# Performance work log

Measured on AMD Instinct MI355X. Metric: run time of the kernel, lower is better.

## Reference

```python
import jax, jax.numpy as jnp
import numpy as np

EPS = 1e-5  # BatchNorm1d default eps


def _uf_death(fv, u, v):
    """0-dim lower-star persistence on a (disjoint-union) graph via union-find.
    fv: [N] vertex filtration values (float np). u, v: [E] endpoints (int np).
    Returns death[N]: index of the vertex whose filtration value is the death
    time of the component born at each vertex (self-index => essential / f,f).
    Edges are processed in order of their lower-star filtration value
    max(fv[u], fv[v]) (stable sort, matching simplex-tree filtration order).
    Elder rule: the component whose birth vertex has larger (f, index) dies.
    """
    N = fv.shape[0]
    fe = np.maximum(fv[u], fv[v])
    order = np.argsort(fe, kind='stable')
    parent = np.arange(N)
    birth = np.arange(N)   # birth vertex of the component rooted here
    death = np.arange(N)   # default: pair (f_v, f_v)

    def find(i):
        r = i
        while parent[r] != r:
            r = parent[r]
        while parent[i] != r:  # path compression
            parent[i], i = r, parent[i]
        return r

    for e in order:
        a, b = int(u[e]), int(v[e])
        ra, rb = find(a), find(b)
        if ra == rb:
            continue
        ba, bb = birth[ra], birth[rb]
        if (fv[ba], ba) <= (fv[bb], bb):
            elder_b, young_b = ba, bb
        else:
            elder_b, young_b = bb, ba
        # death vertex = edge endpoint realizing the edge filtration value
        w = a if (fv[a], a) >= (fv[b], b) else b
        death[young_b] = w
        parent[ra] = rb
        birth[rb] = elder_b
    return death


def _death_indices(x, W1, b1, W2, b2, edge_index):
    """Host-side (numpy) computation of pairing indices. Indices are piecewise
    constant w.r.t. the floats, so gradients do not flow through them."""
    xn = np.asarray(jax.device_get(x), dtype=np.float32)
    fv = np.maximum(xn @ np.asarray(W1) + np.asarray(b1), 0.0) @ np.asarray(W2) + np.asarray(b2)  # [N, F]
    ei = np.asarray(jax.device_get(edge_index))
    u, v = ei[0], ei[1]
    F = fv.shape[1]
    return np.stack([_uf_death(fv[:, k], u, v) for k in range(F)], axis=0)  # [F, N]


def _togl_forward(x, death_idx, batch, num_graphs,
                  W1, b1, W2, b2, W_in, b_in,
                  g1W, g1b, l1W, g2W, g2b, l2W, bn_gamma, bn_beta):
    N = x.shape[0]
    # Filtration MLP: Linear -> ReLU -> Linear
    fv = jnp.maximum(x @ W1 + b1, 0.0) @ W2 + b2          # [N, F]
    births = fv.T                                          # [F, N]
    deaths = jnp.take_along_axis(fv.T, death_idx, axis=1)  # [F, N]
    pd = jnp.stack([births, deaths], axis=-1)              # [F, N, 2]
    # per-node concat over filtrations: [N, 2F]
    x0 = pd.transpose(1, 0, 2).reshape(N, -1)
    x0 = jnp.maximum(x0 @ W_in + b_in, 0.0)                # Linear + ReLU

    def deepset(h, GW, Gb, LW):
        s = jax.ops.segment_sum(h, batch, num_segments=num_graphs)
        c = jax.ops.segment_sum(jnp.ones((h.shape[0], 1), h.dtype), batch,
                                num_segments=num_graphs)
        xm = (s / c) @ LW                                  # Lambda(scatter_mean)
        return h @ GW + Gb - xm[batch]

    x0 = jnp.maximum(deepset(x0, g1W, g1b, l1W), 0.0)      # DeepSet + ReLU
    x0 = deepset(x0, g2W, g2b, l2W)                        # DeepSet -> n_features
    r = jnp.maximum(x0, 0.0)
    mu = r.mean(axis=0)
    var = r.var(axis=0)                                    # biased, as BN training
    y = bn_gamma * (r - mu) * jax.lax.rsqrt(var + EPS) + bn_beta
    return x + y


def setup_inputs() -> dict:
    key = jax.random.key(0)
    ks = jax.random.split(key, 16)
    B, NPG, EPG = 32, 1024, 2048
    N, E = B * NPG, B * EPG
    n_feat, hid, n_filt, out_dim = 512, 512, 8, 64

    rng = np.random.default_rng(0)
    off = np.repeat(np.arange(B, dtype=np.int32) * NPG, EPG)
    u = rng.integers(0, NPG, E).astype(np.int32) + off
    v = rng.integers(0, NPG, E).astype(np.int32) + off
    edge_index = jnp.asarray(np.stack([u, v], axis=0))
    batch = jnp.asarray(np.repeat(np.arange(B, dtype=np.int32), NPG))
    vertex_slices = jnp.asarray(np.arange(B + 1, dtype=np.int32) * NPG)
    edge_slices = jnp.asarray(np.arange(B + 1, dtype=np.int32) * EPG)

    def lin(k, fan_in, shape):
        return jax.random.uniform(k, shape, jnp.float32, -1.0, 1.0) / np.sqrt(fan_in)

    return {
        'x': jax.random.normal(ks[0], (N, n_feat), jnp.float32),
        'edge_index': edge_index,
        'batch': batch,
        'vertex_slices': vertex_slices,
        'edge_slices': edge_slices,
        'W1': lin(ks[1], n_feat, (n_feat, hid)),
        'b1': lin(ks[2], n_feat, (hid,)),
        'W2': lin(ks[3], hid, (hid, n_filt)),
        'b2': lin(ks[4], hid, (n_filt,)),
        'W_in': lin(ks[5], 2 * n_filt, (2 * n_filt, out_dim)),
        'b_in': lin(ks[6], 2 * n_filt, (out_dim,)),
        'g1W': lin(ks[7], out_dim, (out_dim, out_dim)),
        'g1b': lin(ks[8], out_dim, (out_dim,)),
        'l1W': lin(ks[9], out_dim, (out_dim, out_dim)),
        'g2W': lin(ks[10], out_dim, (out_dim, n_feat)),
        'g2b': lin(ks[11], out_dim, (n_feat,)),
        'l2W': lin(ks[12], out_dim, (out_dim, n_feat)),
        'bn_gamma': jnp.ones((n_feat,), jnp.float32),
        'bn_beta': jnp.zeros((n_feat,), jnp.float32),
    }


def reference(x, edge_index, batch, vertex_slices, edge_slices,
              W1, b1, W2, b2, W_in, b_in,
              g1W, g1b, l1W, g2W, g2b, l2W, bn_gamma, bn_beta):
    num_graphs = int(vertex_slices.shape[0]) - 1
    death_idx = jnp.asarray(_death_indices(x, W1, b1, W2, b2, edge_index))  # [F, N]
    return _togl_forward(x, death_idx, batch, num_graphs,
                         W1, b1, W2, b2, W_in, b_in,
                         g1W, g1b, l1W, g2W, g2b, l2W, bn_gamma, bn_beta)
```

## Files before the change

kernel.cpp:

```cpp
#include <hip/hip_runtime.h>
#include <stdint.h>

static constexpr int NN    = 32768;
static constexpr int NPG   = 1024;
static constexpr int EPG   = 2048;
static constexpr int NGR   = 32;
static constexpr int NF    = 8;
static constexpr int FEAT  = 512;
static constexpr int ODIM  = 64;
static constexpr int ETOT  = NGR * EPG;

typedef short bf16x8 __attribute__((ext_vector_type(8)));
typedef float f32x4  __attribute__((ext_vector_type(4)));

__device__ __forceinline__ unsigned int fsort(float f) {
    unsigned int u = __float_as_uint(f);
    return (u & 0x80000000u) ? ~u : (u | 0x80000000u);
}

__device__ __forceinline__ unsigned long long shfl64(unsigned long long x, int src) {
    unsigned int lo = __shfl((unsigned int)x, src);
    unsigned int hi = __shfl((unsigned int)(x >> 32), src);
    return ((unsigned long long)hi << 32) | lo;
}

__device__ __forceinline__ void split2(float a, float b, unsigned& hi, unsigned& lo) {
    unsigned ua = __float_as_uint(a), ub = __float_as_uint(b);
    hi = (ua >> 16) | (ub & 0xffff0000u);
    float ra = a - __uint_as_float(ua & 0xffff0000u);
    float rb = b - __uint_as_float(ub & 0xffff0000u);
    lo = (__float_as_uint(ra) >> 16) | (__float_as_uint(rb) & 0xffff0000u);
}

__global__ __launch_bounds__(256) void w1swz_k(
        const float* __restrict__ W1,
        unsigned short* __restrict__ Whi, unsigned short* __restrict__ Wlo) {
    __shared__ float T[64][65];
    const int tid = threadIdx.x;
    const int kb = blockIdx.x >> 3, cb = blockIdx.x & 7;
    const int r16 = tid >> 4, c4 = tid & 15;
#pragma unroll
    for (int p = 0; p < 4; ++p) {
        int kl = r16 + p * 16;
        *(float4*)&T[kl][c4 * 4] = *(const float4*)&W1[(size_t)(kb * 64 + kl) * FEAT + cb * 64 + c4 * 4];
    }
    __syncthreads();
    const int col_l = tid >> 2;
    const int col = cb * 64 + col_l;
    const int sw = (col + (col >> 2)) & 3;
#pragma unroll
    for (int q = 0; q < 2; ++q) {
        int ch = (tid & 3) + q * 4;
        int ktl = ch >> 2, slot = ch & 3;
        int koff = slot ^ sw;
        unsigned hi[4], lo[4];
#pragma unroll
        for (int pj = 0; pj < 4; ++pj) {
            float a = T[ktl * 32 + koff * 8 + pj * 2 + 0][col_l];
            float b = T[ktl * 32 + koff * 8 + pj * 2 + 1][col_l];
            split2(a, b, hi[pj], lo[pj]);
        }
        size_t o = (size_t)col * 512 + (size_t)kb * 64 + ktl * 32 + slot * 8;
        *(uint4*)&Whi[o] = make_uint4(hi[0], hi[1], hi[2], hi[3]);
        *(uint4*)&Wlo[o] = make_uint4(lo[0], lo[1], lo[2], lo[3]);
    }
}

__global__ __launch_bounds__(256, 2) void mfma_fv_k(
        const float* __restrict__ x, const unsigned short* __restrict__ Whi,
        const unsigned short* __restrict__ Wlo, const float* __restrict__ b1,
        const float* __restrict__ W2, float* __restrict__ fvpart) {
    __shared__ unsigned short AsHi[4096], AsLo[4096], BsHi[4096], BsLo[4096];
    __shared__ float W2s[128][8];
    __shared__ float b1s[128];

    const int tid = threadIdx.x;
    const int lane = tid & 63, wid = tid >> 6;
    const int wr = wid >> 1, wc = wid & 1;
    const int b = blockIdx.x;
    const int rb = (b & 7) * 32 + (b >> 5);
    const int cb = (b >> 3) & 3;
    const int rowBase = rb * 128, colBase = cb * 128;

    for (int i = tid; i < 1024; i += 256)
        W2s[i >> 3][i & 7] = W2[(size_t)(colBase + (i >> 3)) * NF + (i & 7)];
    if (tid < 128) b1s[tid] = b1[colBase + tid];

    const int arow = tid >> 1, ah2 = tid & 1;
    const int aswz = (arow + (arow >> 2)) & 3;
    const float* xp = x + (size_t)(rowBase + arow) * FEAT + ah2 * 16;
    const int bcol = tid >> 1;
    const size_t bsrc = (size_t)(colBase + bcol) * 512 + (size_t)(tid & 1) * 16;
    const int bdst = bcol * 32 + (tid & 1) * 16;

    f32x4 acc[4][4];
#pragma unroll
    for (int m = 0; m < 4; ++m)
#pragma unroll
        for (int n = 0; n < 4; ++n) acc[m][n] = (f32x4){0.f, 0.f, 0.f, 0.f};

    float4 av[4];
    uint4 bhv[2], blv[2];
    av[0] = ((const float4*)xp)[0]; av[1] = ((const float4*)xp)[1];
    av[2] = ((const float4*)xp)[2]; av[3] = ((const float4*)xp)[3];
    bhv[0] = *(const uint4*)(Whi + bsrc); bhv[1] = *(const uint4*)(Whi + bsrc + 8);
    blv[0] = *(const uint4*)(Wlo + bsrc); blv[1] = *(const uint4*)(Wlo + bsrc + 8);

    for (int tk = 0; tk < 16; ++tk) {
        __syncthreads();
#pragma unroll
        for (int cj = 0; cj < 2; ++cj) {
            int koff = ah2 * 2 + cj;
            int slot = koff ^ aswz;
            unsigned h0, h1, h2, h3, l0, l1, l2, l3;
            split2(av[cj * 2 + 0].x, av[cj * 2 + 0].y, h0, l0);
            split2(av[cj * 2 + 0].z, av[cj * 2 + 0].w, h1, l1);
            split2(av[cj * 2 + 1].x, av[cj * 2 + 1].y, h2, l2);
            split2(av[cj * 2 + 1].z, av[cj * 2 + 1].w, h3, l3);
            int o = arow * 32 + slot * 8;
            *(uint4*)&AsHi[o] = make_uint4(h0, h1, h2, h3);
            *(uint4*)&AsLo[o] = make_uint4(l0, l1, l2, l3);
        }
        *(uint4*)&BsHi[bdst] = bhv[0]; *(uint4*)&BsHi[bdst + 8] = bhv[1];
        *(uint4*)&BsLo[bdst] = blv[0]; *(uint4*)&BsLo[bdst + 8] = blv[1];
        if (tk < 15) {
            const float* xq = xp + (tk + 1) * 32;
            av[0] = ((const float4*)xq)[0]; av[1] = ((const float4*)xq)[1];
            av[2] = ((const float4*)xq)[2]; av[3] = ((const float4*)xq)[3];
            const unsigned short* bh = Whi + bsrc + (size_t)(tk + 1) * 32;
            const unsigned short* bl = Wlo + bsrc + (size_t)(tk + 1) * 32;
            bhv[0] = *(const uint4*)bh; bhv[1] = *(const uint4*)(bh + 8);
            blv[0] = *(const uint4*)bl; blv[1] = *(const uint4*)(bl + 8);
        }
        __syncthreads();
        bf16x8 fa[4], fb[4], f2[4];
#pragma unroll
        for (int m = 0; m < 4; ++m) {
            int r = wr * 64 + m * 16 + (lane & 15);
            int slot = (lane >> 4) ^ ((r + (r >> 2)) & 3);
            fa[m] = *(const bf16x8*)&AsHi[r * 32 + slot * 8];
        }
#pragma unroll
        for (int n = 0; n < 4; ++n) {
            int c = wc * 64 + n * 16 + (lane & 15);
            int slot = (lane >> 4) ^ ((c + (c >> 2)) & 3);
            fb[n] = *(const bf16x8*)&BsHi[c * 32 + slot * 8];
        }
#pragma unroll
        for (int m = 0; m < 4; ++m)
#pragma unroll
            for (int n = 0; n < 4; ++n)
                acc[m][n] = __builtin_amdgcn_mfma_f32_16x16x32_bf16(fa[m], fb[n], acc[m][n], 0, 0, 0);
#pragma unroll
        for (int n = 0; n < 4; ++n) {
            int c = wc * 64 + n * 16 + (lane & 15);
            int slot = (lane >> 4) ^ ((c + (c >> 2)) & 3);
            f2[n] = *(const bf16x8*)&BsLo[c * 32 + slot * 8];
        }
#pragma unroll
        for (int m = 0; m < 4; ++m)
#pragma unroll
            for (int n = 0; n < 4; ++n)
                acc[m][n] = __builtin_amdgcn_mfma_f32_16x16x32_bf16(fa[m], f2[n], acc[m][n], 0, 0, 0);
#pragma unroll
        for (int m = 0; m < 4; ++m) {
            int r = wr * 64 + m * 16 + (lane & 15);
            int slot = (lane >> 4) ^ ((r + (r >> 2)) & 3);
            f2[m] = *(const bf16x8*)&AsLo[r * 32 + slot * 8];
        }
#pragma unroll
        for (int m = 0; m < 4; ++m)
#pragma unroll
            for (int n = 0; n < 4; ++n)
                acc[m][n] = __builtin_amdgcn_mfma_f32_16x16x32_bf16(f2[m], fb[n], acc[m][n], 0, 0, 0);
    }

    const int p = cb * 2 + wc;
#pragma unroll
    for (int m = 0; m < 4; ++m) {
        float pf[4][8];
#pragma unroll
        for (int r = 0; r < 4; ++r)
#pragma unroll
            for (int j = 0; j < 8; ++j) pf[r][j] = 0.f;
#pragma unroll
        for (int n = 0; n < 4; ++n) {
            int c = wc * 64 + n * 16 + (lane & 15);
            float bc = b1s[c];
            float4 wA = *(const float4*)&W2s[c][0];
            float4 wB = *(const float4*)&W2s[c][4];
#pragma unroll
            for (int r = 0; r < 4; ++r) {
                float h = fmaxf(acc[m][n][r] + bc, 0.f);
                pf[r][0] += h * wA.x; pf[r][1] += h * wA.y; pf[r][2] += h * wA.z; pf[r][3] += h * wA.w;
                pf[r][4] += h * wB.x; pf[r][5] += h * wB.y; pf[r][6] += h * wB.z; pf[r][7] += h * wB.w;
            }
        }
#pragma unroll
        for (int mask = 1; mask <= 8; mask <<= 1)
#pragma unroll
            for (int r = 0; r < 4; ++r)
#pragma unroll
                for (int j = 0; j < 8; ++j) pf[r][j] += __shfl_xor(pf[r][j], mask);
        if ((lane & 15) == 0) {
            int rowb = rowBase + wr * 64 + m * 16 + (lane >> 4) * 4;
#pragma unroll
            for (int r = 0; r < 4; ++r) {
                *(float4*)&fvpart[(((size_t)p << 15) + rowb + r) * NF + 0] =
                    make_float4(pf[r][0], pf[r][1], pf[r][2], pf[r][3]);
                *(float4*)&fvpart[(((size_t)p << 15) + rowb + r) * NF + 4] =
                    make_float4(pf[r][4], pf[r][5], pf[r][6], pf[r][7]);
            }
        }
    }
}

__global__ __launch_bounds__(256) void fvred_k(
        const float* __restrict__ fvpart, const float* __restrict__ b2,
        float* __restrict__ fv, float* __restrict__ fvT) {
    const int row = blockIdx.x * 256 + threadIdx.x;
    float s[8];
    *(float4*)&s[0] = *(const float4*)&b2[0];
    *(float4*)&s[4] = *(const float4*)&b2[4];
#pragma unroll
    for (int p = 0; p < 8; ++p) {
        float4 lo = *(const float4*)&fvpart[(((size_t)p << 15) + row) * NF + 0];
        float4 hi = *(const float4*)&fvpart[(((size_t)p << 15) + row) * NF + 4];
        s[0] += lo.x; s[1] += lo.y; s[2] += lo.z; s[3] += lo.w;
        s[4] += hi.x; s[5] += hi.y; s[6] += hi.z; s[7] += hi.w;
    }
    *(float4*)&fv[(size_t)row * NF + 0] = *(float4*)&s[0];
    *(float4*)&fv[(size_t)row * NF + 4] = *(float4*)&s[4];
#pragma unroll
    for (int j = 0; j < 8; ++j) fvT[(size_t)j * NN + row] = s[j];
}

__global__ __launch_bounds__(512) void uf_sort_k(
        const float* __restrict__ fvT, const int* __restrict__ ei,
        unsigned int* __restrict__ suvw) {
    __shared__ float fvl[NPG];
    __shared__ unsigned long long keys[EPG];
    __shared__ unsigned int uvw[EPG];
    const int tid = threadIdx.x;
    const int g = blockIdx.x >> 3, k = blockIdx.x & 7;

    for (int i = tid; i < NPG; i += 512) fvl[i] = fvT[(size_t)k * NN + (g << 10) + i];
    __syncthreads();
    for (int e = tid; e < EPG; e += 512) {
        int eg = g * EPG + e;
        int u = ei[eg] & (NPG - 1);
        int v = ei[ETOT + eg] & (NPG - 1);
        unsigned int fku = fsort(fvl[u]);
        unsigned int fkv = fsort(fvl[v]);
        unsigned int wfl = (fku > fkv || (fku == fkv && u >= v)) ? 1u : 0u;
        unsigned int fe = fku > fkv ? fku : fkv;
        uvw[e] = (unsigned)u | ((unsigned)v << 10) | (wfl << 20);
        keys[e] = ((unsigned long long)fe << 32) | (unsigned)e;
    }
    for (int size = 2; size <= EPG; size <<= 1) {
        for (int stride = size >> 1; stride > 0; stride >>= 1) {
            __syncthreads();
            for (int i = tid; i < EPG; i += 512) {
                int j = i ^ stride;
                if (j > i) {
                    unsigned long long a = keys[i], b = keys[j];
                    bool asc = (i & size) == 0;
                    if (asc ? (a > b) : (a < b)) { keys[i] = b; keys[j] = a; }
                }
            }
        }
    }
    __syncthreads();
    for (int i = tid; i < EPG; i += 512)
        suvw[(size_t)blockIdx.x * EPG + i] = uvw[(unsigned)(keys[i] & 0xffffffffULL)];
}

__global__ __launch_bounds__(256) void uf_merge_k(
        const float* __restrict__ fvT, const unsigned int* __restrict__ suvw,
        float* __restrict__ dvT) {
    __shared__ float fvl[NPG];
    __shared__ unsigned long long node[NPG];
    __shared__ unsigned short deathl[NPG];
    __shared__ unsigned int se[EPG];

    const int tid = threadIdx.x;
    const int g = blockIdx.x >> 3, k = blockIdx.x & 7;

    for (int i = tid; i < NPG; i += 256) {
        float val = fvT[(size_t)k * NN + (g << 10) + i];
        fvl[i] = val;
        node[i] = ((unsigned long long)fsort(val) << 32) | ((unsigned long long)(unsigned)i << 16) | (unsigned)i;
        deathl[i] = (unsigned short)i;
    }
    for (int i = tid; i < EPG / 4; i += 256)
        ((uint4*)se)[i] = ((const uint4*)(suvw + (size_t)blockIdx.x * EPG))[i];
    __syncthreads();

    if (tid < 64) {
        const int lane = tid;
        volatile unsigned int* vn32 = (volatile unsigned int*)node;
        volatile unsigned long long* vn64 = (volatile unsigned long long*)node;
        for (int w = 0; w < EPG / 64; ++w) {
            unsigned int pk = se[w * 64 + lane];
            int u = (int)(pk & 1023u), v = (int)((pk >> 10) & 1023u);
            int wd = ((pk >> 20) & 1u) ? u : v;
            int ru = u;
            {
                unsigned int lw = vn32[ru * 2];
                int p = (int)(lw & 0xffffu);
                while (p != ru) {
                    unsigned int lw2 = vn32[p * 2];
                    int gp = (int)(lw2 & 0xffffu);
                    if (gp != p) vn32[ru * 2] = (lw & 0xffff0000u) | (unsigned)gp;
                    ru = p; lw = lw2; p = gp;
                }
            }
            int rv = v;
            {
                unsigned int lw = vn32[rv * 2];
                int p = (int)(lw & 0xffffu);
                while (p != rv) {
                    unsigned int lw2 = vn32[p * 2];
                    int gp = (int)(lw2 & 0xffffu);
                    if (gp != p) vn32[rv * 2] = (lw & 0xffff0000u) | (unsigned)gp;
                    rv = p; lw = lw2; p = gp;
                }
            }
            unsigned long long wa = vn64[ru];
            unsigned long long wb = vn64[rv];
            bool aliveF = (ru != rv);
            unsigned long long mask = __ballot(aliveF);
            while (mask) {
                int li = (int)__builtin_ctzll(mask);
                int bru = __shfl(ru, li), brv = __shfl(rv, li);
                unsigned long long bwa = shfl64(wa, li), bwb = shfl64(wb, li);
                int bw = __shfl(wd, li);
                bool uE = (bwa >> 16) <= (bwb >> 16);
                int rE = uE ? bru : brv;
                int rY = uE ? brv : bru;
                unsigned long long wE = uE ? bwa : bwb;
                unsigned long long wY = uE ? bwb : bwa;
                if (lane == li) {
                    deathl[(int)((wY >> 16) & 0xffffu)] = (unsigned short)bw;
                    vn64[rY] = (wY & ~0xffffULL) | (unsigned)rE;
                }
                if (ru == rY) { ru = rE; wa = wE; }
                if (rv == rY) { rv = rE; wb = wE; }
                aliveF = aliveF && (lane > li) && (ru != rv);
                mask = __ballot(aliveF);
            }
            __builtin_amdgcn_wave_barrier();
        }
    }
    __syncthreads();
    for (int i = tid; i < NPG; i += 256)
        dvT[(size_t)k * NN + (g << 10) + i] = fvl[deathl[i]];
}

__global__ __launch_bounds__(256, 2) void feat_k(
        const float* __restrict__ fv, const float* __restrict__ dvT,
        const float* __restrict__ W_in, const float* __restrict__ b_in,
        float* __restrict__ h0) {
    __shared__ float Ws[16][64];
    __shared__ float bs[64];
    const int tid = threadIdx.x;
    for (int i = tid; i < 1024; i += 256) Ws[i >> 6][i & 63] = W_in[i];
    if (tid < 64) bs[tid] = b_in[tid];
    __syncthreads();
    const int n = blockIdx.x * 256 + tid;
    float4 f0 = *(const float4*)&fv[(size_t)n * NF + 0];
    float4 f1 = *(const float4*)&fv[(size_t)n * NF + 4];
    float dd[8];
#pragma unroll
    for (int j = 0; j < 8; ++j) dd[j] = dvT[(size_t)j * NN + n];
    float x0[16] = { f0.x, dd[0], f0.y, dd[1], f0.z, dd[2], f0.w, dd[3],
                     f1.x, dd[4], f1.y, dd[5], f1.z, dd[6], f1.w, dd[7] };
    float out[64];
#pragma unroll
    for (int j = 0; j < 64; ++j) out[j] = bs[j];
#pragma unroll
    for (int i = 0; i < 16; ++i) {
        float a = x0[i];
#pragma unroll
        for (int j4 = 0; j4 < 16; ++j4) {
            float4 w = *(const float4*)&Ws[i][j4 * 4];
            out[j4 * 4 + 0] += a * w.x; out[j4 * 4 + 1] += a * w.y;
            out[j4 * 4 + 2] += a * w.z; out[j4 * 4 + 3] += a * w.w;
        }
    }
#pragma unroll
    for (int j4 = 0; j4 < 16; ++j4) {
        float4 o = { fmaxf(out[j4 * 4 + 0], 0.f), fmaxf(out[j4 * 4 + 1], 0.f),
                     fmaxf(out[j4 * 4 + 2], 0.f), fmaxf(out[j4 * 4 + 3], 0.f) };
        *(float4*)&h0[(size_t)n * 64 + j4 * 4] = o;
    }
}

__global__ void reduce64_k(const float* __restrict__ h, float* __restrict__ s) {
    __shared__ float part[4][64];
    const int tid = threadIdx.x, g = blockIdx.x;
    const int c = tid & 63, rg = tid >> 6;
    float acc = 0.f;
    for (int r = rg; r < NPG; r += 4) acc += h[(size_t)(g * NPG + r) * 64 + c];
    part[rg][c] = acc;
    __syncthreads();
    if (tid < 64) s[g * 64 + tid] = part[0][tid] + part[1][tid] + part[2][tid] + part[3][tid];
}

__global__ void lam_k(const float* __restrict__ s, const float* __restrict__ LW,
                      const float* __restrict__ Gb, float* __restrict__ bias, int Fout) {
    __shared__ float sg[64];
    const int tid = threadIdx.x, g = blockIdx.x;
    if (tid < 64) sg[tid] = s[g * 64 + tid] * (1.0f / 1024.0f);
    __syncthreads();
    for (int j = tid; j < Fout; j += 256) {
        float acc = 0.f;
        for (int i = 0; i < 64; ++i) acc += sg[i] * LW[i * Fout + j];
        bias[g * Fout + j] = Gb[j] - acc;
    }
}

__global__ __launch_bounds__(256, 2) void ds1_k(
        const float* __restrict__ h0, const float* __restrict__ g1W,
        const float* __restrict__ bias1, float* __restrict__ h1) {
    __shared__ float Ws[64][64];
    const int tid = threadIdx.x;
    for (int i = tid; i < 4096; i += 256) Ws[i >> 6][i & 63] = g1W[i];
    __syncthreads();
    const int n = blockIdx.x * 256 + tid;
    const int g = n >> 10;
    float in[64];
#pragma unroll
    for (int i4 = 0; i4 < 16; ++i4) {
        float4 t = *(const float4*)&h0[(size_t)n * 64 + i4 * 4];
        in[i4 * 4 + 0] = t.x; in[i4 * 4 + 1] = t.y; in[i4 * 4 + 2] = t.z; in[i4 * 4 + 3] = t.w;
    }
    float out[64];
#pragma unroll
    for (int j4 = 0; j4 < 16; ++j4) {
        float4 b = *(const float4*)&bias1[g * 64 + j4 * 4];
        out[j4 * 4 + 0] = b.x; out[j4 * 4 + 1] = b.y; out[j4 * 4 + 2] = b.z; out[j4 * 4 + 3] = b.w;
    }
#pragma unroll 8
    for (int i = 0; i < 64; ++i) {
        float a = in[i];
#pragma unroll
        for (int j4 = 0; j4 < 16; ++j4) {
            float4 w = *(const float4*)&Ws[i][j4 * 4];
            out[j4 * 4 + 0] += a * w.x; out[j4 * 4 + 1] += a * w.y;
            out[j4 * 4 + 2] += a * w.z; out[j4 * 4 + 3] += a * w.w;
        }
    }
#pragma unroll
    for (int j4 = 0; j4 < 16; ++j4) {
        float4 o = { fmaxf(out[j4 * 4 + 0], 0.f), fmaxf(out[j4 * 4 + 1], 0.f),
                     fmaxf(out[j4 * 4 + 2], 0.f), fmaxf(out[j4 * 4 + 3], 0.f) };
        *(float4*)&h1[(size_t)n * 64 + j4 * 4] = o;
    }
}

__global__ __launch_bounds__(256, 2) void ds2_k(
        const float* __restrict__ h1, const float* __restrict__ g2W,
        const float* __restrict__ bias2, float* __restrict__ rout) {
    __shared__ float Ht[32][68];
    __shared__ float Wt[64][68];
    const int tid = threadIdx.x;
    const int rowBase = blockIdx.x * 32;
    const int g = rowBase >> 10;
#pragma unroll
    for (int p = 0; p < 2; ++p) {
        int fid = tid + p * 256;
        int r = fid >> 4, c4 = fid & 15;
        *(float4*)&Ht[r][c4 * 4] = *(const float4*)&h1[(size_t)(rowBase + r) * 64 + c4 * 4];
    }
    const int cg = tid & 15, rg = tid >> 4;
    for (int nc = 0; nc < 8; ++nc) {
        __syncthreads();
#pragma unroll
        for (int p = 0; p < 4; ++p) {
            int fid = tid + p * 256;
            int kk = fid >> 4, c4 = fid & 15;
            *(float4*)&Wt[kk][c4 * 4] = *(const float4*)&g2W[(size_t)kk * FEAT + nc * 64 + c4 * 4];
        }
        __syncthreads();
        float a0[4] = {0.f, 0.f, 0.f, 0.f}, a1[4] = {0.f, 0.f, 0.f, 0.f};
#pragma unroll 8
        for (int kk = 0; kk < 64; ++kk) {
            float h0v = Ht[rg * 2][kk], h1v = Ht[rg * 2 + 1][kk];
            float4 w = *(const float4*)&Wt[kk][cg * 4];
            a0[0] += h0v * w.x; a0[1] += h0v * w.y; a0[2] += h0v * w.z; a0[3] += h0v * w.w;
            a1[0] += h1v * w.x; a1[1] += h1v * w.y; a1[2] += h1v * w.z; a1[3] += h1v * w.w;
        }
        float4 bv = *(const float4*)&bias2[g * FEAT + nc * 64 + cg * 4];
        int row0 = rowBase + rg * 2;
        float4 o0 = { fmaxf(a0[0] + bv.x, 0.f), fmaxf(a0[1] + bv.y, 0.f),
                      fmaxf(a0[2] + bv.z, 0.f), fmaxf(a0[3] + bv.w, 0.f) };
        float4 o1 = { fmaxf(a1[0] + bv.x, 0.f), fmaxf(a1[1] + bv.y, 0.f),
                      fmaxf(a1[2] + bv.z, 0.f), fmaxf(a1[3] + bv.w, 0.f) };
        *(float4*)&rout[(size_t)row0 * FEAT + nc * 64 + cg * 4] = o0;
        *(float4*)&rout[(size_t)(row0 + 1) * FEAT + nc * 64 + cg * 4] = o1;
    }
}

__global__ void bnst1_k(const float* __restrict__ r, float* __restrict__ psum, float* __restrict__ psq) {
    const int tid = threadIdx.x, b = blockIdx.x;
    const int row0 = b * 128;
    float s0 = 0.f, q0 = 0.f, s1 = 0.f, q1 = 0.f;
    for (int rr = 0; rr < 128; ++rr) {
        float a = r[(size_t)(row0 + rr) * FEAT + tid];
        float c = r[(size_t)(row0 + rr) * FEAT + 256 + tid];
        s0 += a; q0 += a * a; s1 += c; q1 += c * c;
    }
    psum[b * FEAT + tid] = s0; psum[b * FEAT + 256 + tid] = s1;
    psq [b * FEAT + tid] = q0; psq [b * FEAT + 256 + tid] = q1;
}

__global__ void bnst2_k(const float* __restrict__ psum, const float* __restrict__ psq,
                        const float* __restrict__ gamma, const float* __restrict__ beta,
                        float* __restrict__ scsh) {
    const int tid = threadIdx.x;
    for (int c = tid; c < FEAT; c += 256) {
        float s = 0.f, q = 0.f;
        for (int b = 0; b < 256; ++b) { s += psum[b * FEAT + c]; q += psq[b * FEAT + c]; }
        float mu = s * (1.0f / (float)NN);
        float var = q * (1.0f / (float)NN) - mu * mu;
        float sc = gamma[c] * rsqrtf(var + 1e-5f);
        scsh[c] = sc;
        scsh[FEAT + c] = beta[c] - mu * sc;
    }
}

__global__ void final_k(const float* __restrict__ x, const float* __restrict__ scsh,
                        float* __restrict__ out) {
    const int total4 = NN * (FEAT / 4);
    for (int idx = blockIdx.x * 256 + threadIdx.x; idx < total4; idx += 2048 * 256) {
        int col4 = idx & (FEAT / 4 - 1);
        float4 rv = *(float4*)&out[(size_t)idx * 4];
        float4 xv = *(const float4*)&x[(size_t)idx * 4];
        float4 sc = *(const float4*)&scsh[col4 * 4];
        float4 sh = *(const float4*)&scsh[FEAT + col4 * 4];
        float4 o = { xv.x + rv.x * sc.x + sh.x, xv.y + rv.y * sc.y + sh.y,
                     xv.z + rv.z * sc.z + sh.z, xv.w + rv.w * sc.w + sh.w };
        *(float4*)&out[(size_t)idx * 4] = o;
    }
}

extern "C" void kernel_launch(void* const* d_in, const int* in_sizes, int n_in,
                              void* d_out, int out_size, void* d_ws, size_t ws_size,
                              hipStream_t stream) {
    const float* x     = (const float*)d_in[0];
    const int*   ei    = (const int*)d_in[1];
    const float* W1    = (const float*)d_in[5];
    const float* b1    = (const float*)d_in[6];
    const float* W2    = (const float*)d_in[7];
    const float* b2    = (const float*)d_in[8];
    const float* W_in  = (const float*)d_in[9];
    const float* b_in  = (const float*)d_in[10];
    const float* g1W   = (const float*)d_in[11];
    const float* g1b   = (const float*)d_in[12];
    const float* l1W   = (const float*)d_in[13];
    const float* g2W   = (const float*)d_in[14];
    const float* g2b   = (const float*)d_in[15];
    const float* l2W   = (const float*)d_in[16];
    const float* gamma = (const float*)d_in[17];
    const float* beta  = (const float*)d_in[18];
    float* out = (float*)d_out;
    float* ws  = (float*)d_ws;

    float* fv    = ws;
    float* dvT   = ws + 262144;
    float* h0    = ws + 524288;
    float* h1    = ws + 2621440;
    unsigned short* W1hi = (unsigned short*)(ws + 262144);
    unsigned short* W1lo = (unsigned short*)(ws + 393216);
    float*        fvpart = ws + 524288;
    float*        fvT  = ws + 2621440;
    unsigned int* suvw = (unsigned int*)(ws + 2883584);
    float* s1    = ws + 4718592;
    float* bias1 = ws + 4720640;
    float* s2    = ws + 4722688;
    float* bias2 = ws + 4724736;
    float* psum  = ws + 4741120;
    float* psq   = ws + 4872192;
    float* scsh  = ws + 5003264;

    hipLaunchKernelGGL(w1swz_k,    dim3(64),   dim3(256), 0, stream, W1, W1hi, W1lo);
    hipLaunchKernelGGL(mfma_fv_k,  dim3(1024), dim3(256), 0, stream, x, W1hi, W1lo, b1, W2, fvpart);
    hipLaunchKernelGGL(fvred_k,    dim3(128),  dim3(256), 0, stream, fvpart, b2, fv, fvT);
    hipLaunchKernelGGL(uf_sort_k,  dim3(256),  dim3(512), 0, stream, fvT, ei, suvw);
    hipLaunchKernelGGL(uf_merge_k, dim3(256),  dim3(256), 0, stream, fvT, suvw, dvT);
    hipLaunchKernelGGL(feat_k,     dim3(128),  dim3(256), 0, stream, fv, dvT, W_in, b_in, h0);
    hipLaunchKernelGGL(reduce64_k, dim3(32),   dim3(256), 0, stream, h0, s1);
    hipLaunchKernelGGL(lam_k,      dim3(32),   dim3(256), 0, stream, s1, l1W, g1b, bias1, 64);
    hipLaunchKernelGGL(ds1_k,      dim3(128),  dim3(256), 0, stream, h0, g1W, bias1, h1);
    hipLaunchKernelGGL(reduce64_k, dim3(32),   dim3(256), 0, stream, h1, s2);
    hipLaunchKernelGGL(lam_k,      dim3(32),   dim3(256), 0, stream, s2, l2W, g2b, bias2, 512);
    hipLaunchKernelGGL(ds2_k,      dim3(1024), dim3(256), 0, stream, h1, g2W, bias2, out);
    hipLaunchKernelGGL(bnst1_k,    dim3(256),  dim3(256), 0, stream, out, psum, psq);
    hipLaunchKernelGGL(bnst2_k,    dim3(1),    dim3(256), 0, stream, psum, psq, gamma, beta, scsh);
    hipLaunchKernelGGL(final_k,    dim3(2048), dim3(256), 0, stream, x, scsh, out);
}
```

Baseline: 685.8 us.

## Parallelize union-find merges within a wave using per-root claim arbitration

Replaces the serial per-lane merge loop (ballot, then broadcast one alive edge at a time) with a round-based scheme. In each round, every alive lane claims its younger root through an atomicMin in shared memory. Lanes that win their claim and come before the first blocked lane commit their merges together, and the rest re-run find and try again. This aims to cut the number of serialized shuffle iterations per 64-edge chunk, at the cost of extra atomics, fences and repeated root finds.

```diff
diff --git a/kernel.cpp b/kernel.cpp
--- a/kernel.cpp
+++ b/kernel.cpp
@@ -16,12 +16,6 @@
 __device__ __forceinline__ unsigned int fsort(float f) {
     unsigned int u = __float_as_uint(f);
     return (u & 0x80000000u) ? ~u : (u | 0x80000000u);
-}
-
-__device__ __forceinline__ unsigned long long shfl64(unsigned long long x, int src) {
-    unsigned int lo = __shfl((unsigned int)x, src);
-    unsigned int hi = __shfl((unsigned int)(x >> 32), src);
-    return ((unsigned long long)hi << 32) | lo;
 }
 
 __device__ __forceinline__ void split2(float a, float b, unsigned& hi, unsigned& lo) {
@@ -282,6 +276,7 @@
     __shared__ unsigned long long node[NPG];
     __shared__ unsigned short deathl[NPG];
     __shared__ unsigned int se[EPG];
+    __shared__ unsigned int claim[NPG];
 
     const int tid = threadIdx.x;
     const int g = blockIdx.x >> 3, k = blockIdx.x & 7;
@@ -291,6 +286,7 @@
         fvl[i] = val;
         node[i] = ((unsigned long long)fsort(val) << 32) | ((unsigned long long)(unsigned)i << 16) | (unsigned)i;
         deathl[i] = (unsigned short)i;
+        claim[i] = ~0u;
     }
     for (int i = tid; i < EPG / 4; i += 256)
         ((uint4*)se)[i] = ((const uint4*)(suvw + (size_t)blockIdx.x * EPG))[i];
@@ -300,6 +296,7 @@
         const int lane = tid;
         volatile unsigned int* vn32 = (volatile unsigned int*)node;
         volatile unsigned long long* vn64 = (volatile unsigned long long*)node;
+        volatile unsigned int* vcl = (volatile unsigned int*)claim;
         for (int w = 0; w < EPG / 64; ++w) {
             unsigned int pk = se[w * 64 + lane];
             int u = (int)(pk & 1023u), v = (int)((pk >> 10) & 1023u);
@@ -328,26 +325,53 @@
             }
             unsigned long long wa = vn64[ru];
             unsigned long long wb = vn64[rv];
-            bool aliveF = (ru != rv);
-            unsigned long long mask = __ballot(aliveF);
-            while (mask) {
-                int li = (int)__builtin_ctzll(mask);
-                int bru = __shfl(ru, li), brv = __shfl(rv, li);
-                unsigned long long bwa = shfl64(wa, li), bwb = shfl64(wb, li);
-                int bw = __shfl(wd, li);
-                bool uE = (bwa >> 16) <= (bwb >> 16);
-                int rE = uE ? bru : brv;
-                int rY = uE ? brv : bru;
-                unsigned long long wE = uE ? bwa : bwb;
-                unsigned long long wY = uE ? bwb : bwa;
-                if (lane == li) {
-                    deathl[(int)((wY >> 16) & 0xffffu)] = (unsigned short)bw;
-                    vn64[rY] = (wY & ~0xffffULL) | (unsigned)rE;
+            bool alive = (ru != rv);
+            while (__ballot(alive)) {
+                bool wasAlive = alive;
+                int ry = 0, re = 0;
+                unsigned long long wy = 0;
+                if (alive) {
+                    bool uY = (wa >> 16) > (wb >> 16);
+                    ry = uY ? ru : rv; re = uY ? rv : ru;
+                    wy = uY ? wa : wb;
+                    atomicMin(&claim[ry], (unsigned)lane);
                 }
-                if (ru == rY) { ru = rE; wa = wE; }
-                if (rv == rY) { rv = rE; wb = wE; }
-                aliveF = aliveF && (lane > li) && (ru != rv);
-                mask = __ballot(aliveF);
+                __threadfence_block();
+                bool win0 = alive && (vcl[ry] == (unsigned)lane);
+                unsigned long long blockedM = __ballot(alive && !win0);
+                int fb = blockedM ? (int)__builtin_ctzll(blockedM) : 64;
+                bool win = win0 && (lane < fb);
+                if (win) {
+                    deathl[(int)((wy >> 16) & 0xffffu)] = (unsigned short)wd;
+                    vn64[ry] = (wy & ~0xffffULL) | (unsigned)re;
+                    alive = false;
+                }
+                __threadfence_block();
+                if (wasAlive) vcl[ry] = ~0u;
+                if (alive) {
+                    int r = ru;
+                    unsigned int lw = vn32[r * 2];
+                    int p = (int)(lw & 0xffffu);
+                    while (p != r) {
+                        unsigned int lw2 = vn32[p * 2];
+                        int gp = (int)(lw2 & 0xffffu);
+                        if (gp != p) vn32[r * 2] = (lw & 0xffff0000u) | (unsigned)gp;
+                        r = p; lw = lw2; p = gp;
+                    }
+                    ru = r;
+                    r = rv;
+                    lw = vn32[r * 2];
+                    p = (int)(lw & 0xffffu);
+                    while (p != r) {
+                        unsigned int lw2 = vn32[p * 2];
+                        int gp = (int)(lw2 & 0xffffu);
+                        if (gp != p) vn32[r * 2] = (lw & 0xffff0000u) | (unsigned)gp;
+                        r = p; lw = lw2; p = gp;
+                    }
+                    rv = r;
+                    wa = vn64[ru]; wb = vn64[rv];
+                    alive = (ru != rv);
+                }
             }
             __builtin_amdgcn_wave_barrier();
         }
```

New measurement: 816.2 us. +19.0%, slower.
